# Performance work log

Measured on AMD Instinct MI355X. Metric: run time of the kernel, lower is better.

## Reference

```python
import jax, jax.numpy as jnp
import numpy as np

IN_C, HID_C, OUT_C = 6, 128, 6
B, H, W = 8, 256, 256


def _make_weight(key, oc, ic):
    return jax.random.normal(key, (oc, ic, 5), dtype=jnp.float32) / np.sqrt(ic * 5)


def setup_inputs() -> dict:
    key = jax.random.key(0)
    ks = jax.random.split(key, 5)
    x = jax.random.normal(ks[0], (B, IN_C, H, W), dtype=jnp.float32)
    return {
        "x": x,
        "w1": _make_weight(ks[1], HID_C, IN_C),
        "b1": jnp.zeros((HID_C,), jnp.float32),
        "w2": _make_weight(ks[2], HID_C, HID_C),
        "b2": jnp.zeros((HID_C,), jnp.float32),
        "w3": _make_weight(ks[3], HID_C, HID_C),
        "b3": jnp.zeros((HID_C,), jnp.float32),
        "w4": _make_weight(ks[4], OUT_C, HID_C),
        "b4": jnp.zeros((OUT_C,), jnp.float32),
    }


def cross_conv(x, w, b):
    # w: [oc, ic, 5] -> dense 3x3 kernel with 5-point cross stencil
    oc, ic, _ = w.shape
    k = jnp.zeros((oc, ic, 3, 3), dtype=w.dtype)
    k = k.at[:, :, 1, 1].set(w[:, :, 0])  # center
    k = k.at[:, :, 0, 1].set(w[:, :, 1])  # up
    k = k.at[:, :, 2, 1].set(w[:, :, 2])  # down
    k = k.at[:, :, 1, 0].set(w[:, :, 3])  # left
    k = k.at[:, :, 1, 2].set(w[:, :, 4])  # right
    y = jax.lax.conv_general_dilated(
        x, k, window_strides=(1, 1), padding="SAME",
        dimension_numbers=("NCHW", "OIHW", "NCHW"))
    return y + b[None, :, None, None]


def reference(x, w1, b1, w2, b2, w3, b3, w4, b4):
    h = jax.nn.relu(cross_conv(x, w1, b1))
    h = jax.nn.relu(cross_conv(h, w2, b2))
    h = jax.nn.relu(cross_conv(h, w3, b3))
    return cross_conv(h, w4, b4)
```

## Files before the change

### kernel.cpp

```cpp
#include <hip/hip_runtime.h>


#define BB   8
#define HH   256
#define WW   256

typedef _Float16 f16x8 __attribute__((ext_vector_type(8)));
typedef float    f32x4 __attribute__((ext_vector_type(4)));

__device__ _Float16 W1g[128 * 32];
__device__ _Float16 W2g[20 * 128 * 32];
__device__ _Float16 W3g[20 * 128 * 32];
__device__ _Float16 W4g[5 * 16 * 128];

__global__ void prep(const float* __restrict__ w1, const float* __restrict__ w2,
                     const float* __restrict__ w3, const float* __restrict__ w4)
{
    int idx = blockIdx.x * 256 + threadIdx.x;
    if (idx < 81920) {
        int icb = idx & 31, oc = (idx >> 5) & 127, ks = idx >> 12;
        int tap = ks >> 2, ic = (ks & 3) * 32 + icb;
        W2g[idx] = (_Float16)w2[(oc * 128 + ic) * 5 + tap];
    } else if (idx < 163840) {
        int k = idx - 81920;
        int icb = k & 31, oc = (k >> 5) & 127, ks = k >> 12;
        int tap = ks >> 2, ic = (ks & 3) * 32 + icb;
        W3g[k] = (_Float16)w3[(oc * 128 + ic) * 5 + tap];
    } else if (idx < 174080) {
        int k = idx - 163840;
        int t = k / 2048, oc = (k >> 7) & 15, ic = k & 127;
        W4g[k] = (_Float16)((oc < 6) ? w4[(oc * 128 + ic) * 5 + t] : 0.f);
    } else if (idx < 178176) {
        int k = idx - 174080;
        int kk = k & 31, oc = k >> 5;
        float v = 0.f;
        if (kk < 30) {
            int tap = (kk * 43) >> 8;
            int ic = kk - 6 * tap;
            v = w1[(oc * 6 + ic) * 5 + tap];
        }
        W1g[k] = (_Float16)v;
    }
}

__global__ __launch_bounds__(256, 3) void g1(
    const float* __restrict__ x, const float* __restrict__ bias,
    _Float16* __restrict__ outp)
{
    __shared__ _Float16 Ap[128 * 40];
    const int tid = threadIdx.x;
    const int j0 = blockIdx.x * 16, i0 = blockIdx.y * 8, b = blockIdx.z;
    const int px = tid & 127, half = tid >> 7;
    const int pr = px >> 4, pp = px & 15;
#pragma unroll
    for (int it = 0; it < 16; ++it) {
        int k = it * 2 + half;
        float v = 0.f;
        if (k < 30) {
            int tap = (k * 43) >> 8, ic = k - 6 * tap;
            int di = (tap == 1) ? -1 : ((tap == 2) ? 1 : 0);
            int dj = (tap == 3) ? -1 : ((tap == 4) ? 1 : 0);
            int gi = i0 + pr + di, gj = j0 + pp + dj;
            if (((unsigned)gi < 256u) && ((unsigned)gj < 256u))
                v = x[(((size_t)b * 6 + ic) * 256 + gi) * 256 + gj];
        }
        Ap[px * 40 + k] = (_Float16)v;
    }
    __syncthreads();

    const int lane = tid & 63, w = tid >> 6, l16 = lane & 15, quad = lane >> 4;
    f32x4 acc[2][8] = {};
    f16x8 a0 = *(const f16x8*)&Ap[((2 * w + 0) * 16 + l16) * 40 + quad * 8];
    f16x8 a1 = *(const f16x8*)&Ap[((2 * w + 1) * 16 + l16) * 40 + quad * 8];
#pragma unroll
    for (int nf = 0; nf < 8; ++nf) {
        f16x8 bf = *(const f16x8*)&W1g[(nf * 16 + l16) * 32 + quad * 8];
        acc[0][nf] = __builtin_amdgcn_mfma_f32_16x16x32_f16(a0, bf, acc[0][nf], 0, 0, 0);
        acc[1][nf] = __builtin_amdgcn_mfma_f32_16x16x32_f16(a1, bf, acc[1][nf], 0, 0, 0);
    }
#pragma unroll
    for (int mf = 0; mf < 2; ++mf) {
        const size_t rowb = ((size_t)b * 256 + i0 + 2 * w + mf) * 256 + j0;
#pragma unroll
        for (int nf = 0; nf < 8; ++nf) {
            const float bv = bias[nf * 16 + l16];
#pragma unroll
            for (int r = 0; r < 4; ++r)
                outp[(rowb + quad * 4 + r) * 128 + nf * 16 + l16] =
                    (_Float16)fmaxf(acc[mf][nf][r] + bv, 0.f);
        }
    }
}

template<int LAYER>
__global__ __launch_bounds__(256, 3) void gmid(
    const _Float16* __restrict__ in, const float* __restrict__ bias,
    _Float16* __restrict__ outp)
{
    const _Float16* wt = (LAYER == 2) ? W2g : W3g;
    __shared__ __align__(16) _Float16 Al[180 * 128];
    const int tid = threadIdx.x;
    const int lane = tid & 63, w = tid >> 6;
    const int j0 = blockIdx.x * 16, i0 = blockIdx.y * 8, b = blockIdx.z;
    const bool top = (blockIdx.y == 0), bot = (blockIdx.y == 31);
    const bool left = (blockIdx.x == 0), right = (blockIdx.x == 15);

    {
        const int pxl = lane & 15;
#pragma unroll
        for (int k = 0; k < 12; ++k) {
            const int m = w + 4 * k;
            if (m < 45) {
                const int s = 4 * m + (lane >> 4);
                const int r = (s * 114) >> 11;
                const int p = s - 18 * r;
                int gi = i0 - 1 + r; gi = gi < 0 ? 0 : (gi > 255 ? 255 : gi);
                int gj = j0 - 1 + p; gj = gj < 0 ? 0 : (gj > 255 ? 255 : gj);
                const _Float16* src = in + (((size_t)(b * 256 + gi)) * 256 + gj) * 128
                                         + ((pxl ^ (s & 7)) << 3);
                __builtin_amdgcn_global_load_lds(
                    (const __attribute__((address_space(1))) void*)src,
                    (__attribute__((address_space(3))) void*)(Al + m * 512),
                    16, 0, 0);
            }
        }
    }
    __syncthreads();
    if (top | bot | left | right) {
#pragma unroll
        for (int pass = 0; pass < 2; ++pass) {
            const int gidx = (tid >> 3) + 32 * pass, c = tid & 7;
            int sid = -1;
            if (gidx < 18)      { if (top)   sid = gidx; }
            else if (gidx < 36) { if (bot)   sid = 162 + gidx - 18; }
            else if (gidx < 46) { if (left)  sid = (gidx - 36) * 18; }
            else if (gidx < 56) { if (right) sid = (gidx - 46) * 18 + 17; }
            if (sid >= 0) {
                const f16x8 z = {};
                *(f16x8*)(Al + sid * 128 + c * 16)     = z;
                *(f16x8*)(Al + sid * 128 + c * 16 + 8) = z;
            }
        }
        __syncthreads();
    }

    const int l16 = lane & 15, quad = lane >> 4;
    const int mg = w & 1, ng = w >> 1;
    const int r0 = mg * 4;
    const int n0 = ng * 64;

    const _Float16* wb = wt + (size_t)(n0 + l16) * 32 + quad * 8;

    f32x4 acc[4][4] = {};
    const int DR[5] = {1, 0, 2, 1, 1}, DP[5] = {1, 1, 1, 0, 2};

    auto lda = [&](int ks, int r) -> f16x8 {
        const int tap = ks >> 2, kc = ks & 3;
        const int s = (DR[tap] + r0 + r) * 18 + DP[tap] + l16;
        const int ch = (kc * 4 + quad) ^ (s & 7);
        return *(const f16x8*)&Al[s * 128 + ch * 8];
    };

    f16x8 bc[4], bn[4], ac[4], an[4];
#pragma unroll
    for (int nf = 0; nf < 4; ++nf) bc[nf] = *(const f16x8*)(wb + nf * 512);
#pragma unroll
    for (int r = 0; r < 4; ++r) ac[r] = lda(0, r);

#pragma unroll
    for (int ks = 0; ks < 20; ++ks) {
        if (ks < 19) {
#pragma unroll
            for (int nf = 0; nf < 4; ++nf)
                bn[nf] = *(const f16x8*)(wb + (size_t)(ks + 1) * 4096 + nf * 512);
#pragma unroll
            for (int r = 0; r < 4; ++r) an[r] = lda(ks + 1, r);
        }
        __builtin_amdgcn_s_setprio(1);
#pragma unroll
        for (int r = 0; r < 4; ++r)
#pragma unroll
            for (int nf = 0; nf < 4; ++nf)
                acc[r][nf] = __builtin_amdgcn_mfma_f32_16x16x32_f16(
                    ac[r], bc[nf], acc[r][nf], 0, 0, 0);
        __builtin_amdgcn_s_setprio(0);
#pragma unroll
        for (int nf = 0; nf < 4; ++nf) bc[nf] = bn[nf];
#pragma unroll
        for (int r = 0; r < 4; ++r) ac[r] = an[r];
    }

#pragma unroll
    for (int r = 0; r < 4; ++r) {
        const size_t rowb = ((size_t)b * 256 + i0 + r0 + r) * 256 + j0;
#pragma unroll
        for (int nf = 0; nf < 4; ++nf) {
            const float bv = bias[n0 + nf * 16 + l16];
#pragma unroll
            for (int vi = 0; vi < 4; ++vi)
                outp[(rowb + quad * 4 + vi) * 128 + n0 + nf * 16 + l16] =
                    (_Float16)fmaxf(acc[r][nf][vi] + bv, 0.f);
        }
    }
}

__global__ __launch_bounds__(256, 3) void g4(
    const _Float16* __restrict__ in, const float* __restrict__ bias,
    float* __restrict__ outp)
{
    __shared__ _Float16 Al[6 * 18 * 136];
    const int tid = threadIdx.x;
    const int jt = blockIdx.x, it = blockIdx.y, b = blockIdx.z;
    const int i0 = it * 4, j0 = jt * 16;

    for (int t = tid; t < 6 * 18 * 16; t += 256) {
        int r = t / 288, rem = t % 288, p = rem >> 4, q = rem & 15;
        int gi = i0 - 1 + r, gj = j0 - 1 + p;
        f16x8 v = {0, 0, 0, 0, 0, 0, 0, 0};
        if (((unsigned)gi < 256u) && ((unsigned)gj < 256u))
            v = *(const f16x8*)&in[(((size_t)b * 256 + gi) * 256 + gj) * 128 + q * 8];
        *(f16x8*)&Al[(r * 18 + p) * 136 + q * 8] = v;
    }
    __syncthreads();

    const int lane = tid & 63, wid = tid >> 6;
    const int l16 = lane & 15, quad = lane >> 4;
    f32x4 acc = {};
    const int DR[5] = {1, 0, 2, 1, 1}, DP[5] = {1, 1, 1, 0, 2};

#pragma unroll
    for (int ks = 0; ks < 20; ++ks) {
        const int tap = ks >> 2, kc = ks & 3;
        const int koff = kc * 32 + quad * 8;
        f16x8 bf = *(const f16x8*)&W4g[(size_t)(tap * 16 + l16) * 128 + koff];
        f16x8 af = *(const f16x8*)&Al[((DR[tap] + wid) * 18 + DP[tap] + l16) * 136 + koff];
        acc = __builtin_amdgcn_mfma_f32_16x16x32_f16(af, bf, acc, 0, 0, 0);
    }

    if (l16 < 6) {
        const float bb = bias[l16];
        const int i = i0 + wid;
#pragma unroll
        for (int vi = 0; vi < 4; ++vi) {
            int jj = j0 + quad * 4 + vi;
            outp[(((size_t)b * 6 + l16) << 16) + i * 256 + jj] = acc[vi] + bb;
        }
    }
}

extern "C" void kernel_launch(void* const* d_in, const int* in_sizes, int n_in,
                              void* d_out, int out_size, void* d_ws, size_t ws_size,
                              hipStream_t stream) {
    const float* x  = (const float*)d_in[0];
    const float* w1 = (const float*)d_in[1];
    const float* b1 = (const float*)d_in[2];
    const float* w2 = (const float*)d_in[3];
    const float* b2 = (const float*)d_in[4];
    const float* w3 = (const float*)d_in[5];
    const float* b3 = (const float*)d_in[6];
    const float* w4 = (const float*)d_in[7];
    const float* b4 = (const float*)d_in[8];
    float* out = (float*)d_out;

    const size_t act = (size_t)BB * HH * WW * 128;
    _Float16* A1 = (_Float16*)d_ws;
    _Float16* A2 = A1 + act;

    prep<<<696, 256, 0, stream>>>(w1, w2, w3, w4);
    dim3 blk(256, 1, 1);
    dim3 gm(16, 32, 8);
    g1<<<gm, blk, 0, stream>>>(x, b1, A1);
    gmid<2><<<gm, blk, 0, stream>>>(A1, b2, A2);
    gmid<3><<<gm, blk, 0, stream>>>(A2, b3, A1);
    g4<<<dim3(16, 64, 8), blk, 0, stream>>>(A1, b4, out);
}
```

Measured before the change: 419.0 us.

## Rework final conv layer with async global-to-LDS loads, XOR swizzle, larger tiles

The last layer now covers 8 rows per block instead of 4, which halves the grid and the redundant halo reloads, and each wave computes two output rows so it reuses the same weight fragment. The halo tile is loaded with global_load_lds direct-to-LDS transfers using clamped addresses and an XOR channel swizzle in place of padding. Border pixels are then zeroed in a second pass that only runs on edge blocks. Setprio is wrapped around the MFMAs. This only touches the smallest layer, so any effect on total time is limited, and the extra sync and edge-zeroing add some complexity.

Result: faster. 390.5 us (-6.8%).

```diff
diff --git a/kernel.cpp b/kernel.cpp
--- a/kernel.cpp
+++ b/kernel.cpp
@@ -208,42 +208,86 @@
     const _Float16* __restrict__ in, const float* __restrict__ bias,
     float* __restrict__ outp)
 {
-    __shared__ _Float16 Al[6 * 18 * 136];
+    __shared__ __align__(16) _Float16 Al[180 * 128];
     const int tid = threadIdx.x;
-    const int jt = blockIdx.x, it = blockIdx.y, b = blockIdx.z;
-    const int i0 = it * 4, j0 = jt * 16;
-
-    for (int t = tid; t < 6 * 18 * 16; t += 256) {
-        int r = t / 288, rem = t % 288, p = rem >> 4, q = rem & 15;
-        int gi = i0 - 1 + r, gj = j0 - 1 + p;
-        f16x8 v = {0, 0, 0, 0, 0, 0, 0, 0};
-        if (((unsigned)gi < 256u) && ((unsigned)gj < 256u))
-            v = *(const f16x8*)&in[(((size_t)b * 256 + gi) * 256 + gj) * 128 + q * 8];
-        *(f16x8*)&Al[(r * 18 + p) * 136 + q * 8] = v;
+    const int lane = tid & 63, w = tid >> 6;
+    const int j0 = blockIdx.x * 16, i0 = blockIdx.y * 8, b = blockIdx.z;
+    const bool top = (blockIdx.y == 0), bot = (blockIdx.y == 31);
+    const bool left = (blockIdx.x == 0), right = (blockIdx.x == 15);
+
+    {
+        const int pxl = lane & 15;
+#pragma unroll
+        for (int k = 0; k < 12; ++k) {
+            const int m = w + 4 * k;
+            if (m < 45) {
+                const int s = 4 * m + (lane >> 4);
+                const int r = (s * 114) >> 11;
+                const int p = s - 18 * r;
+                int gi = i0 - 1 + r; gi = gi < 0 ? 0 : (gi > 255 ? 255 : gi);
+                int gj = j0 - 1 + p; gj = gj < 0 ? 0 : (gj > 255 ? 255 : gj);
+                const _Float16* src = in + (((size_t)(b * 256 + gi)) * 256 + gj) * 128
+                                         + ((pxl ^ (s & 7)) << 3);
+                __builtin_amdgcn_global_load_lds(
+                    (const __attribute__((address_space(1))) void*)src,
+                    (__attribute__((address_space(3))) void*)(Al + m * 512),
+                    16, 0, 0);
+            }
+        }
     }
     __syncthreads();
-
-    const int lane = tid & 63, wid = tid >> 6;
+    if (top | bot | left | right) {
+#pragma unroll
+        for (int pass = 0; pass < 2; ++pass) {
+            const int gidx = (tid >> 3) + 32 * pass, c = tid & 7;
+            int sid = -1;
+            if (gidx < 18)      { if (top)   sid = gidx; }
+            else if (gidx < 36) { if (bot)   sid = 162 + gidx - 18; }
+            else if (gidx < 46) { if (left)  sid = (gidx - 36) * 18; }
+            else if (gidx < 56) { if (right) sid = (gidx - 46) * 18 + 17; }
+            if (sid >= 0) {
+                const f16x8 z = {};
+                *(f16x8*)(Al + sid * 128 + c * 16)     = z;
+                *(f16x8*)(Al + sid * 128 + c * 16 + 8) = z;
+            }
+        }
+        __syncthreads();
+    }
+
     const int l16 = lane & 15, quad = lane >> 4;
-    f32x4 acc = {};
     const int DR[5] = {1, 0, 2, 1, 1}, DP[5] = {1, 1, 1, 0, 2};
 
+    auto lda = [&](int ks, int row) -> f16x8 {
+        const int tap = ks >> 2, kc = ks & 3;
+        const int s = (DR[tap] + row) * 18 + DP[tap] + l16;
+        const int ch = (kc * 4 + quad) ^ (s & 7);
+        return *(const f16x8*)&Al[s * 128 + ch * 8];
+    };
+
+    f32x4 acc[2] = {};
 #pragma unroll
     for (int ks = 0; ks < 20; ++ks) {
         const int tap = ks >> 2, kc = ks & 3;
         const int koff = kc * 32 + quad * 8;
         f16x8 bf = *(const f16x8*)&W4g[(size_t)(tap * 16 + l16) * 128 + koff];
-        f16x8 af = *(const f16x8*)&Al[((DR[tap] + wid) * 18 + DP[tap] + l16) * 136 + koff];
-        acc = __builtin_amdgcn_mfma_f32_16x16x32_f16(af, bf, acc, 0, 0, 0);
+        __builtin_amdgcn_s_setprio(1);
+#pragma unroll
+        for (int f = 0; f < 2; ++f)
+            acc[f] = __builtin_amdgcn_mfma_f32_16x16x32_f16(
+                lda(ks, 2 * w + f), bf, acc[f], 0, 0, 0);
+        __builtin_amdgcn_s_setprio(0);
     }
 
     if (l16 < 6) {
         const float bb = bias[l16];
-        const int i = i0 + wid;
-#pragma unroll
-        for (int vi = 0; vi < 4; ++vi) {
-            int jj = j0 + quad * 4 + vi;
-            outp[(((size_t)b * 6 + l16) << 16) + i * 256 + jj] = acc[vi] + bb;
+#pragma unroll
+        for (int f = 0; f < 2; ++f) {
+            const int i = i0 + 2 * w + f;
+#pragma unroll
+            for (int vi = 0; vi < 4; ++vi) {
+                int jj = j0 + quad * 4 + vi;
+                outp[(((size_t)b * 6 + l16) << 16) + i * 256 + jj] = acc[f][vi] + bb;
+            }
         }
     }
 }
@@ -272,5 +316,5 @@
     g1<<<gm, blk, 0, stream>>>(x, b1, A1);
     gmid<2><<<gm, blk, 0, stream>>>(A1, b2, A2);
     gmid<3><<<gm, blk, 0, stream>>>(A2, b3, A1);
-    g4<<<dim3(16, 64, 8), blk, 0, stream>>>(A1, b4, out);
-}
+    g4<<<gm, blk, 0, stream>>>(A1, b4, out);
+}
```
